# Kernel optimization log

Hardware: AMD Instinct MI355X
Metric: run time of the kernel (lower is better)

The kernel has to match this reference:

```python
import jax, jax.numpy as jnp
import numpy as np

N = 50000
NFEAT = 128
NHID = 64
EPS = 1e-5
NEG_SLOPE = 0.2


def gat_conv(x, src, dst, W, a_src, a_dst, b):
    # x: [N, in], W: [out, in], a_src/a_dst: [out], b: [out]
    h = x @ W.T                                   # [N, out]
    alpha_s = h @ a_src                           # [N]
    alpha_d = h @ a_dst                           # [N]
    e = jax.nn.leaky_relu(alpha_s[src] + alpha_d[dst], NEG_SLOPE)  # [E]
    # segment softmax over destination nodes
    m = jax.ops.segment_max(e, dst, num_segments=N)
    e = jnp.exp(e - m[dst])
    s = jax.ops.segment_sum(e, dst, num_segments=N)
    alpha = e / (s[dst] + 1e-16)
    out = jax.ops.segment_sum(alpha[:, None] * h[src], dst, num_segments=N)
    return out + b


def batch_norm(x, gamma, beta):
    mu = jnp.mean(x, axis=0)
    var = jnp.mean((x - mu) ** 2, axis=0)
    return gamma * (x - mu) * jax.lax.rsqrt(var + EPS) + beta


def setup_inputs() -> dict:
    key = jax.random.key(0)
    ks = jax.random.split(key, 24)
    E = 800000
    x = jax.random.normal(ks[0], (N, NFEAT), dtype=jnp.float32)
    edge_index = jax.random.randint(ks[1], (2, E), 0, N, dtype=jnp.int64)

    def lin(k, o, i):
        return jax.random.normal(k, (o, i), dtype=jnp.float32) / np.sqrt(i)

    def att(k, o):
        return jax.random.normal(k, (o,), dtype=jnp.float32) / np.sqrt(o)

    return dict(
        x=x, edge_index=edge_index,
        W1=lin(ks[2], NHID, NFEAT), a1s=att(ks[3], NHID), a1d=att(ks[4], NHID), b1=jnp.zeros((NHID,), jnp.float32),
        g1=jnp.ones((NHID,), jnp.float32), be1=jnp.zeros((NHID,), jnp.float32),
        W2=lin(ks[5], NHID, NHID), a2s=att(ks[6], NHID), a2d=att(ks[7], NHID), b2=jnp.zeros((NHID,), jnp.float32),
        g2=jnp.ones((NHID,), jnp.float32), be2=jnp.zeros((NHID,), jnp.float32),
        W3=lin(ks[8], NHID, NHID), a3s=att(ks[9], NHID), a3d=att(ks[10], NHID), b3=jnp.zeros((NHID,), jnp.float32),
        g3=jnp.ones((NHID,), jnp.float32), be3=jnp.zeros((NHID,), jnp.float32),
        W4=lin(ks[11], NFEAT, NHID), a4s=att(ks[12], NFEAT), a4d=att(ks[13], NFEAT), b4=jnp.zeros((NFEAT,), jnp.float32),
    )


def reference(x, edge_index, W1, a1s, a1d, b1, g1, be1, W2, a2s, a2d, b2, g2, be2,
              W3, a3s, a3d, b3, g3, be3, W4, a4s, a4d, b4):
    loops = jnp.arange(N, dtype=edge_index.dtype)
    src = jnp.concatenate([edge_index[0], loops])  # add self-loops (PyG default)
    dst = jnp.concatenate([edge_index[1], loops])
    # Encoder
    h = jax.nn.relu(gat_conv(x, src, dst, W1, a1s, a1d, b1))
    h = batch_norm(h, g1, be1)
    h = jax.nn.relu(gat_conv(h, src, dst, W2, a2s, a2d, b2))
    h = batch_norm(h, g2, be2)
    # Attribute decoder
    h = jax.nn.relu(gat_conv(h, src, dst, W3, a3s, a3d, b3))
    h = batch_norm(h, g3, be3)
    x_hat = jax.nn.relu(gat_conv(h, src, dst, W4, a4s, a4d, b4))
    diff = jnp.abs(x - x_hat)
    return diff, x_hat
```

## Files before the change

### kernel.cpp

```cpp
#include <hip/hip_runtime.h>
#include <math.h>

#define NND 50000
#define EPSB 1e-5f
#define SLOPE 0.2f
#define NB 256
#define SBLK 128
#define BRANGE 196

typedef float vfloat4 __attribute__((ext_vector_type(4)));

__device__ __forceinline__ float lrelu(float v) { return v > 0.f ? v : SLOPE * v; }

__device__ __forceinline__ ushort f2bf(float f) {
    unsigned u = __float_as_uint(f);
    unsigned r = (u + 0x7fffu + ((u >> 16) & 1u)) >> 16;
    return (ushort)r;
}

__device__ __forceinline__ void nt_store4(float4 v, float4* p) {
    vfloat4 t = {v.x, v.y, v.z, v.w};
    __builtin_nontemporal_store(t, (vfloat4*)p);
}

__device__ __forceinline__ void acc8(float* a, uint4 w, float e) {
    a[0] += e * __uint_as_float(w.x << 16);
    a[1] += e * __uint_as_float(w.x & 0xffff0000u);
    a[2] += e * __uint_as_float(w.y << 16);
    a[3] += e * __uint_as_float(w.y & 0xffff0000u);
    a[4] += e * __uint_as_float(w.z << 16);
    a[5] += e * __uint_as_float(w.z & 0xffff0000u);
    a[6] += e * __uint_as_float(w.w << 16);
    a[7] += e * __uint_as_float(w.w & 0xffff0000u);
}


__global__ __launch_bounds__(256) void countC_kernel(const int* __restrict__ ei, int E,
                                                     int* __restrict__ cnt, int* __restrict__ C) {
    __shared__ int lc[NB];
    const int tid = threadIdx.x;
    for (int i = tid; i < NB; i += 256) lc[i] = 0;
    __syncthreads();
    const int per = (E + SBLK - 1) / SBLK;
    const int beg = blockIdx.x * per;
    const int end = min(beg + per, E);
    for (int i = beg + tid; i < end; i += 256) {
        int d = __builtin_nontemporal_load(&ei[E + i]);
        atomicAdd(&cnt[d], 1);
        atomicAdd(&lc[d / BRANGE], 1);
    }
    __syncthreads();
    for (int i = tid; i < NB; i += 256) C[i * SBLK + blockIdx.x] = lc[i];
}

__global__ __launch_bounds__(1024) void scanC_kernel(int* __restrict__ C) {
    __shared__ int ps[1024];
    const int t = threadIdx.x;
    int v[NB * SBLK / 1024];
    int s = 0;
#pragma unroll
    for (int j = 0; j < NB * SBLK / 1024; j++) {
        v[j] = C[t * (NB * SBLK / 1024) + j];
        s += v[j];
    }
    ps[t] = s;
    __syncthreads();
    for (int off = 1; off < 1024; off <<= 1) {
        int x = (t >= off) ? ps[t - off] : 0;
        __syncthreads();
        ps[t] += x;
        __syncthreads();
    }
    int ex = ps[t] - s;
#pragma unroll
    for (int j = 0; j < NB * SBLK / 1024; j++) {
        int tmp = v[j];
        C[t * (NB * SBLK / 1024) + j] = ex;
        ex += tmp;
    }
}

__global__ __launch_bounds__(256) void scatter_pairs_kernel(const int* __restrict__ ei, int E,
                                                            const int* __restrict__ C,
                                                            unsigned long long* __restrict__ pairs) {
    __shared__ int woff[NB];
    const int tid = threadIdx.x;
    for (int i = tid; i < NB; i += 256) woff[i] = C[i * SBLK + blockIdx.x];
    __syncthreads();
    const int per = (E + SBLK - 1) / SBLK;
    const int beg = blockIdx.x * per;
    const int end = min(beg + per, E);
    for (int i = beg + tid; i < end; i += 256) {
        int s = __builtin_nontemporal_load(&ei[i]);
        int d = __builtin_nontemporal_load(&ei[E + i]);
        int p = atomicAdd(&woff[d / BRANGE], 1);
        pairs[p] = ((unsigned long long)(unsigned)d << 32) | (unsigned)s;
    }
}

__global__ void scan1_kernel(const int* __restrict__ in, int n, int* __restrict__ outex,
                             int* __restrict__ bsum) {
    __shared__ int tmp[256];
    int tid = threadIdx.x;
    int i = blockIdx.x * 256 + tid;
    int v = (i < n) ? in[i] + 1 : 0;
    tmp[tid] = v;
    __syncthreads();
    for (int off = 1; off < 256; off <<= 1) {
        int t = (tid >= off) ? tmp[tid - off] : 0;
        __syncthreads();
        tmp[tid] += t;
        __syncthreads();
    }
    if (i < n) outex[i] = tmp[tid] - v;
    if (tid == 255) bsum[blockIdx.x] = tmp[255];
}

__global__ void scan2_kernel(const int* __restrict__ in, int n, int* __restrict__ outex) {
    __shared__ int tmp[256];
    int tid = threadIdx.x;
    int v = (tid < n) ? in[tid] : 0;
    tmp[tid] = v;
    __syncthreads();
    for (int off = 1; off < 256; off <<= 1) {
        int t = (tid >= off) ? tmp[tid - off] : 0;
        __syncthreads();
        tmp[tid] += t;
        __syncthreads();
    }
    if (tid < n) outex[tid] = tmp[tid] - v;
}

__global__ void scan3_kernel(int* __restrict__ rp, const int* __restrict__ boff,
                             int* __restrict__ fill, int* __restrict__ srcs, int n, int etot) {
    int i = blockIdx.x * 256 + threadIdx.x;
    if (i < n) {
        int v = rp[i] + boff[blockIdx.x];
        rp[i] = v;
        srcs[v] = i;
        fill[i] = v + 1;
    }
    if (i == 0) rp[n] = etot;
}

__global__ __launch_bounds__(256) void bucket_csr_kernel(const unsigned long long* __restrict__ pairs,
                                                         int E, const int* __restrict__ C,
                                                         int* __restrict__ fill,
                                                         int* __restrict__ srcs) {
    const int b = blockIdx.x;
    const int beg = C[b * SBLK];
    const int end = (b == NB - 1) ? E : C[(b + 1) * SBLK];
    for (int i = beg + threadIdx.x; i < end; i += 256) {
        unsigned long long pr = __builtin_nontemporal_load(&pairs[i]);
        int d = (int)(pr >> 32);
        int s = (int)(pr & 0xffffffffu);
        int p = atomicAdd(&fill[d], 1);
        srcs[p] = s;
    }
}


template <int K, int FOUT>
__global__ __launch_bounds__(256) void gemm_kernel(
    const float* __restrict__ X, const float* __restrict__ W, ushort* __restrict__ H, int n,
    const float* __restrict__ bnsum, const float* __restrict__ bnsq, const float* __restrict__ g,
    const float* __restrict__ be, const float* __restrict__ asrc, const float* __restrict__ adst,
    float* __restrict__ as_o, float* __restrict__ ad_o) {
    constexpr int SW = FOUT + 4;
    constexpr int SX = 68;
    constexpr int NF = FOUT / 64;
    __shared__ float Wt[64 * SW];
    __shared__ float Xt[64 * SX];
    __shared__ float bnsc[K];
    __shared__ float bnsh[K];
    const int tid = threadIdx.x;
    const int nodeBase = blockIdx.x * 64;
    const int tx = tid & 15, ty = tid >> 4;
    const bool doBN = (bnsum != nullptr);

    if (doBN) {
        const float invn = 1.f / (float)NND;
        for (int f = tid; f < K; f += 256) {
            float mu = bnsum[f] * invn;
            float var = bnsq[f] * invn - mu * mu;
            float r = rsqrtf(var + EPSB);
            float sc = g[f] * r;
            bnsc[f] = sc;
            bnsh[f] = be[f] - mu * sc;
        }
    }
    __syncthreads();

    float acc[4][4 * NF];
#pragma unroll
    for (int i = 0; i < 4; i++)
#pragma unroll
        for (int j = 0; j < 4 * NF; j++) acc[i][j] = 0.f;

    for (int kc = 0; kc < K; kc += 64) {
        for (int idx = tid; idx < FOUT * 64; idx += 256) {
            int f = idx >> 6, kk = idx & 63;
            Wt[kk * SW + f] = W[f * K + kc + kk];
        }
        for (int idx = tid; idx < 64 * 16; idx += 256) {
            int r = idx >> 4, c4 = idx & 15;
            int node = nodeBase + r;
            float4 v = make_float4(0.f, 0.f, 0.f, 0.f);
            if (node < n) {
                v = ((const float4*)X)[node * (K / 4) + (kc >> 2) + c4];
                if (doBN) {
                    int f = kc + c4 * 4;
                    v.x = v.x * bnsc[f + 0] + bnsh[f + 0];
                    v.y = v.y * bnsc[f + 1] + bnsh[f + 1];
                    v.z = v.z * bnsc[f + 2] + bnsh[f + 2];
                    v.w = v.w * bnsc[f + 3] + bnsh[f + 3];
                }
            }
            Xt[(c4 * 4 + 0) * SX + r] = v.x;
            Xt[(c4 * 4 + 1) * SX + r] = v.y;
            Xt[(c4 * 4 + 2) * SX + r] = v.z;
            Xt[(c4 * 4 + 3) * SX + r] = v.w;
        }
        __syncthreads();
#pragma unroll 16
        for (int k = 0; k < 64; k++) {
            const float4 xv = *(const float4*)(Xt + k * SX + ty * 4);
            const float4 wv = *(const float4*)(Wt + k * SW + tx * 4);
            const float xa[4] = {xv.x, xv.y, xv.z, xv.w};
            float wa[4 * NF];
            wa[0] = wv.x; wa[1] = wv.y; wa[2] = wv.z; wa[3] = wv.w;
            if constexpr (NF == 2) {
                const float4 wv2 = *(const float4*)(Wt + k * SW + 64 + tx * 4);
                wa[4] = wv2.x; wa[5] = wv2.y; wa[6] = wv2.z; wa[7] = wv2.w;
            }
#pragma unroll
            for (int i = 0; i < 4; i++)
#pragma unroll
                for (int j = 0; j < 4 * NF; j++) acc[i][j] += xa[i] * wa[j];
        }
        __syncthreads();
    }
#pragma unroll
    for (int i = 0; i < 4; i++) {
        int node = nodeBase + ty * 4 + i;
        if (node < n) {
            ushort4 o;
            o.x = f2bf(acc[i][0]); o.y = f2bf(acc[i][1]);
            o.z = f2bf(acc[i][2]); o.w = f2bf(acc[i][3]);
            ((ushort4*)H)[node * (FOUT / 4) + tx] = o;
            if constexpr (NF == 2) {
                ushort4 o2;
                o2.x = f2bf(acc[i][4]); o2.y = f2bf(acc[i][5]);
                o2.z = f2bf(acc[i][6]); o2.w = f2bf(acc[i][7]);
                ((ushort4*)H)[node * (FOUT / 4) + 16 + tx] = o2;
            }
        }
    }
    if (as_o) {
        float asv[4 * NF], adv[4 * NF];
#pragma unroll
        for (int j = 0; j < 4; j++) {
            asv[j] = asrc[tx * 4 + j];
            adv[j] = adst[tx * 4 + j];
            if constexpr (NF == 2) {
                asv[4 + j] = asrc[64 + tx * 4 + j];
                adv[4 + j] = adst[64 + tx * 4 + j];
            }
        }
#pragma unroll
        for (int i = 0; i < 4; i++) {
            int node = nodeBase + ty * 4 + i;
            float ps = 0.f, pd = 0.f;
#pragma unroll
            for (int j = 0; j < 4 * NF; j++) {
                ps += acc[i][j] * asv[j];
                pd += acc[i][j] * adv[j];
            }
#pragma unroll
            for (int off = 1; off < 16; off <<= 1) {
                ps += __shfl_xor(ps, off, 64);
                pd += __shfl_xor(pd, off, 64);
            }
            if (tx == 0 && node < n) {
                as_o[node] = ps;
                ad_o[node] = pd;
            }
        }
    }
}


template <int F, bool FINAL>
__global__ __launch_bounds__(256) void edge_kernel(
    const int* __restrict__ rp, const int* __restrict__ srcs, const float* __restrict__ as_,
    const float* __restrict__ ad_, const ushort* __restrict__ h, const float* __restrict__ bias,
    float* __restrict__ y, float* __restrict__ bnsum, float* __restrict__ bnsq,
    const float* __restrict__ xin, float* __restrict__ odiff, float* __restrict__ oxhat) {
    constexpr int GS = F / 8;
    constexpr int GPW = 64 / GS;
    const int tid = threadIdx.x;
    const int lane = tid & 63;
    const int wslot = tid >> 6;
    const int sub = lane & (GS - 1);
    const int grp = (blockIdx.x * 4 + wslot) * GPW + lane / GS;
    const int ngrp = gridDim.x * 4 * GPW;
    const float4 bA = ((const float4*)bias)[sub * 2];
    const float4 bB = ((const float4*)bias)[sub * 2 + 1];
    float st[8], qt[8];
#pragma unroll
    for (int j = 0; j < 8; j++) st[j] = qt[j] = 0.f;

    for (int row = grp; row < NND; row += ngrp) {
        const int beg = rp[row], end = rp[row + 1];
        const float ad = ad_[row];
        float a[8];
#pragma unroll
        for (int j = 0; j < 8; j++) a[j] = 0.f;
        float sw = 0.f;
        int i = beg;
        for (; i + 4 <= end; i += 4) {
            int s0 = __builtin_nontemporal_load(&srcs[i]);
            int s1 = __builtin_nontemporal_load(&srcs[i + 1]);
            int s2 = __builtin_nontemporal_load(&srcs[i + 2]);
            int s3 = __builtin_nontemporal_load(&srcs[i + 3]);
            uint4 h0 = *(const uint4*)(h + (size_t)s0 * F + sub * 8);
            uint4 h1 = *(const uint4*)(h + (size_t)s1 * F + sub * 8);
            uint4 h2 = *(const uint4*)(h + (size_t)s2 * F + sub * 8);
            uint4 h3 = *(const uint4*)(h + (size_t)s3 * F + sub * 8);
            float e0 = __expf(fminf(lrelu(as_[s0] + ad), 80.f));
            float e1 = __expf(fminf(lrelu(as_[s1] + ad), 80.f));
            float e2 = __expf(fminf(lrelu(as_[s2] + ad), 80.f));
            float e3 = __expf(fminf(lrelu(as_[s3] + ad), 80.f));
            acc8(a, h0, e0);
            acc8(a, h1, e1);
            acc8(a, h2, e2);
            acc8(a, h3, e3);
            sw += (e0 + e1) + (e2 + e3);
        }
        for (; i < end; i++) {
            int s0 = __builtin_nontemporal_load(&srcs[i]);
            uint4 h0 = *(const uint4*)(h + (size_t)s0 * F + sub * 8);
            float e0 = __expf(fminf(lrelu(as_[s0] + ad), 80.f));
            acc8(a, h0, e0);
            sw += e0;
        }
        const float inv = 1.f / (sw + 1e-16f);
        float4 ya, yb;
        ya.x = fmaxf(a[0] * inv + bA.x, 0.f);
        ya.y = fmaxf(a[1] * inv + bA.y, 0.f);
        ya.z = fmaxf(a[2] * inv + bA.z, 0.f);
        ya.w = fmaxf(a[3] * inv + bA.w, 0.f);
        yb.x = fmaxf(a[4] * inv + bB.x, 0.f);
        yb.y = fmaxf(a[5] * inv + bB.y, 0.f);
        yb.z = fmaxf(a[6] * inv + bB.z, 0.f);
        yb.w = fmaxf(a[7] * inv + bB.w, 0.f);
        if constexpr (FINAL) {
            const float4* xr = (const float4*)(xin + (size_t)row * F);
            float4 xa = xr[sub * 2], xb = xr[sub * 2 + 1];
            float4* xo = (float4*)(oxhat + (size_t)row * F);
            nt_store4(ya, &xo[sub * 2]);
            nt_store4(yb, &xo[sub * 2 + 1]);
            float4 da, db;
            da.x = fabsf(xa.x - ya.x); da.y = fabsf(xa.y - ya.y);
            da.z = fabsf(xa.z - ya.z); da.w = fabsf(xa.w - ya.w);
            db.x = fabsf(xb.x - yb.x); db.y = fabsf(xb.y - yb.y);
            db.z = fabsf(xb.z - yb.z); db.w = fabsf(xb.w - yb.w);
            float4* dio = (float4*)(odiff + (size_t)row * F);
            nt_store4(da, &dio[sub * 2]);
            nt_store4(db, &dio[sub * 2 + 1]);
        } else {
            float4* yo = (float4*)(y + (size_t)row * F);
            nt_store4(ya, &yo[sub * 2]);
            nt_store4(yb, &yo[sub * 2 + 1]);
            st[0] += ya.x; qt[0] += ya.x * ya.x;
            st[1] += ya.y; qt[1] += ya.y * ya.y;
            st[2] += ya.z; qt[2] += ya.z * ya.z;
            st[3] += ya.w; qt[3] += ya.w * ya.w;
            st[4] += yb.x; qt[4] += yb.x * yb.x;
            st[5] += yb.y; qt[5] += yb.y * yb.y;
            st[6] += yb.z; qt[6] += yb.z * yb.z;
            st[7] += yb.w; qt[7] += yb.w * yb.w;
        }
    }
    if constexpr (!FINAL) {
        __shared__ float redS[256][8];
        __shared__ float redQ[256][8];
#pragma unroll
        for (int j = 0; j < 8; j++) {
            redS[tid][j] = st[j];
            redQ[tid][j] = qt[j];
        }
        __syncthreads();
        if (tid < F) {
            int sb = tid >> 3, j = tid & 7;
            float ts = 0.f, tq = 0.f;
            for (int k = 0; k < 256 / GS; k++) {
                int t2 = k * GS + sb;
                ts += redS[t2][j];
                tq += redQ[t2][j];
            }
            atomicAdd(&bnsum[tid], ts);
            atomicAdd(&bnsq[tid], tq);
        }
    }
}


extern "C" void kernel_launch(void* const* d_in, const int* in_sizes, int n_in, void* d_out,
                              int out_size, void* d_ws, size_t ws_size, hipStream_t stream) {
    const float* x = (const float*)d_in[0];
    const int* ei = (const int*)d_in[1];
    const int E = in_sizes[1] / 2;
    const float* W1 = (const float*)d_in[2];
    const float* a1s = (const float*)d_in[3];
    const float* a1d = (const float*)d_in[4];
    const float* b1 = (const float*)d_in[5];
    const float* g1 = (const float*)d_in[6];
    const float* be1 = (const float*)d_in[7];
    const float* W2 = (const float*)d_in[8];
    const float* a2s = (const float*)d_in[9];
    const float* a2d = (const float*)d_in[10];
    const float* b2 = (const float*)d_in[11];
    const float* g2 = (const float*)d_in[12];
    const float* be2 = (const float*)d_in[13];
    const float* W3 = (const float*)d_in[14];
    const float* a3s = (const float*)d_in[15];
    const float* a3d = (const float*)d_in[16];
    const float* b3 = (const float*)d_in[17];
    const float* g3 = (const float*)d_in[18];
    const float* be3 = (const float*)d_in[19];
    const float* W4 = (const float*)d_in[20];
    const float* a4s = (const float*)d_in[21];
    const float* a4d = (const float*)d_in[22];
    const float* b4 = (const float*)d_in[23];

    const int Etot = E + NND;

    char* w = (char*)d_ws;
    auto alloc = [&](size_t bytes) {
        void* p = (void*)w;
        w += (bytes + 255) & ~(size_t)255;
        return p;
    };
    int* cnt = (int*)alloc((size_t)NND * 4);
    float* stats = (float*)alloc(384 * 4);
    int* rp = (int*)alloc((size_t)(NND + 1) * 4);
    int* fill = (int*)alloc((size_t)NND * 4);
    int* bsum = (int*)alloc(256 * 4);
    int* bsum2 = (int*)alloc(256 * 4);
    int* C = (int*)alloc((size_t)NB * SBLK * 4);
    unsigned long long* pairs = (unsigned long long*)alloc((size_t)E * 8);
    int* srcs = (int*)alloc((size_t)Etot * 4);
    ushort* bufH = (ushort*)alloc((size_t)NND * 128 * 2);
    float* bufY = (float*)alloc((size_t)NND * 64 * 4);
    float* asb = (float*)alloc((size_t)NND * 4);
    float* adb = (float*)alloc((size_t)NND * 4);

    const int nblk = (NND + 255) / 256;
    const int ggrid = (NND + 63) / 64;
    const int xgrid = 2048;

    hipError_t _e = hipMemsetAsync(cnt, 0, (((size_t)NND * 4 + 255) & ~(size_t)255) + 384 * 4, stream);
    (void)_e;

    countC_kernel<<<SBLK, 256, 0, stream>>>(ei, E, cnt, C);
    scan1_kernel<<<nblk, 256, 0, stream>>>(cnt, NND, rp, bsum);
    scan2_kernel<<<1, 256, 0, stream>>>(bsum, nblk, bsum2);
    scan3_kernel<<<nblk, 256, 0, stream>>>(rp, bsum2, fill, srcs, NND, Etot);
    scanC_kernel<<<1, 1024, 0, stream>>>(C);
    scatter_pairs_kernel<<<SBLK, 256, 0, stream>>>(ei, E, C, pairs);
    bucket_csr_kernel<<<NB, 256, 0, stream>>>(pairs, E, C, fill, srcs);

    gemm_kernel<128, 64><<<ggrid, 256, 0, stream>>>(x, W1, bufH, NND, nullptr, nullptr, nullptr,
                                                    nullptr, a1s, a1d, asb, adb);
    edge_kernel<64, false><<<xgrid, 256, 0, stream>>>(rp, srcs, asb, adb, bufH, b1, bufY,
                                                      stats + 0, stats + 64, nullptr, nullptr,
                                                      nullptr);
    gemm_kernel<64, 64><<<ggrid, 256, 0, stream>>>(bufY, W2, bufH, NND, stats + 0, stats + 64,
                                                   g1, be1, a2s, a2d, asb, adb);
    edge_kernel<64, false><<<xgrid, 256, 0, stream>>>(rp, srcs, asb, adb, bufH, b2, bufY,
                                                      stats + 128, stats + 192, nullptr, nullptr,
                                                      nullptr);
    gemm_kernel<64, 64><<<ggrid, 256, 0, stream>>>(bufY, W3, bufH, NND, stats + 128, stats + 192,
                                                   g2, be2, a3s, a3d, asb, adb);
    edge_kernel<64, false><<<xgrid, 256, 0, stream>>>(rp, srcs, asb, adb, bufH, b3, bufY,
                                                      stats + 256, stats + 320, nullptr, nullptr,
                                                      nullptr);
    float* odiff = (float*)d_out;
    float* oxhat = (float*)d_out + (size_t)NND * 128;
    gemm_kernel<64, 128><<<ggrid, 256, 0, stream>>>(bufY, W4, bufH, NND, stats + 256, stats + 320,
                                                    g3, be3, a4s, a4d, asb, adb);
    edge_kernel<128, true><<<xgrid, 256, 0, stream>>>(rp, srcs, asb, adb, bufH, b4, nullptr,
                                                      nullptr, nullptr, x, odiff, oxhat);
}
```

Baseline: 547.6 us.

## Drop nontemporal hints, replace memset with zero kernel, halve edge grid

Non-temporal loads of the CSR source indices and non-temporal stores of activations and outputs become ordinary cached accesses. The hipMemsetAsync is replaced by a small custom kernel that zeroes the counts and BN stats, and the edge kernel grid drops from 2048 to 1024 blocks. Bounds clamps are added to the scatter write positions as a safety guard. The changes trade streaming cache hints for normal caching, cut launch and API overhead, and reduce per-block reduction overhead, at the cost of less latency hiding in the edge kernel.

Measured after the change: 454.0 us. -17.1%, faster.

```diff
diff --git a/kernel.cpp b/kernel.cpp
--- a/kernel.cpp
+++ b/kernel.cpp
@@ -8,19 +8,12 @@
 #define SBLK 128
 #define BRANGE 196
 
-typedef float vfloat4 __attribute__((ext_vector_type(4)));
-
 __device__ __forceinline__ float lrelu(float v) { return v > 0.f ? v : SLOPE * v; }
 
 __device__ __forceinline__ ushort f2bf(float f) {
     unsigned u = __float_as_uint(f);
     unsigned r = (u + 0x7fffu + ((u >> 16) & 1u)) >> 16;
     return (ushort)r;
-}
-
-__device__ __forceinline__ void nt_store4(float4 v, float4* p) {
-    vfloat4 t = {v.x, v.y, v.z, v.w};
-    __builtin_nontemporal_store(t, (vfloat4*)p);
 }
 
 __device__ __forceinline__ void acc8(float* a, uint4 w, float e) {
@@ -34,6 +27,12 @@
     a[7] += e * __uint_as_float(w.w & 0xffff0000u);
 }
 
+__global__ void zero_kernel(int* __restrict__ cnt, float* __restrict__ stats) {
+    int i = blockIdx.x * 256 + threadIdx.x;
+    if (i < NND) cnt[i] = 0;
+    if (i < 384) stats[i] = 0.f;
+}
+
 
 __global__ __launch_bounds__(256) void countC_kernel(const int* __restrict__ ei, int E,
                                                      int* __restrict__ cnt, int* __restrict__ C) {
@@ -94,6 +93,7 @@
         int s = __builtin_nontemporal_load(&ei[i]);
         int d = __builtin_nontemporal_load(&ei[E + i]);
         int p = atomicAdd(&woff[d / BRANGE], 1);
+        p = min(p, E - 1);
         pairs[p] = ((unsigned long long)(unsigned)d << 32) | (unsigned)s;
     }
 }
@@ -144,7 +144,7 @@
 }
 
 __global__ __launch_bounds__(256) void bucket_csr_kernel(const unsigned long long* __restrict__ pairs,
-                                                         int E, const int* __restrict__ C,
+                                                         int E, int etot, const int* __restrict__ C,
                                                          int* __restrict__ fill,
                                                          int* __restrict__ srcs) {
     const int b = blockIdx.x;
@@ -155,6 +155,7 @@
         int d = (int)(pr >> 32);
         int s = (int)(pr & 0xffffffffu);
         int p = atomicAdd(&fill[d], 1);
+        p = min(p, etot - 1);
         srcs[p] = s;
     }
 }
@@ -319,10 +320,7 @@
         float sw = 0.f;
         int i = beg;
         for (; i + 4 <= end; i += 4) {
-            int s0 = __builtin_nontemporal_load(&srcs[i]);
-            int s1 = __builtin_nontemporal_load(&srcs[i + 1]);
-            int s2 = __builtin_nontemporal_load(&srcs[i + 2]);
-            int s3 = __builtin_nontemporal_load(&srcs[i + 3]);
+            int s0 = srcs[i], s1 = srcs[i + 1], s2 = srcs[i + 2], s3 = srcs[i + 3];
             uint4 h0 = *(const uint4*)(h + (size_t)s0 * F + sub * 8);
             uint4 h1 = *(const uint4*)(h + (size_t)s1 * F + sub * 8);
             uint4 h2 = *(const uint4*)(h + (size_t)s2 * F + sub * 8);
@@ -338,7 +336,7 @@
             sw += (e0 + e1) + (e2 + e3);
         }
         for (; i < end; i++) {
-            int s0 = __builtin_nontemporal_load(&srcs[i]);
+            int s0 = srcs[i];
             uint4 h0 = *(const uint4*)(h + (size_t)s0 * F + sub * 8);
             float e0 = __expf(fminf(lrelu(as_[s0] + ad), 80.f));
             acc8(a, h0, e0);
@@ -358,20 +356,20 @@
             const float4* xr = (const float4*)(xin + (size_t)row * F);
             float4 xa = xr[sub * 2], xb = xr[sub * 2 + 1];
             float4* xo = (float4*)(oxhat + (size_t)row * F);
-            nt_store4(ya, &xo[sub * 2]);
-            nt_store4(yb, &xo[sub * 2 + 1]);
+            xo[sub * 2] = ya;
+            xo[sub * 2 + 1] = yb;
             float4 da, db;
             da.x = fabsf(xa.x - ya.x); da.y = fabsf(xa.y - ya.y);
             da.z = fabsf(xa.z - ya.z); da.w = fabsf(xa.w - ya.w);
             db.x = fabsf(xb.x - yb.x); db.y = fabsf(xb.y - yb.y);
             db.z = fabsf(xb.z - yb.z); db.w = fabsf(xb.w - yb.w);
             float4* dio = (float4*)(odiff + (size_t)row * F);
-            nt_store4(da, &dio[sub * 2]);
-            nt_store4(db, &dio[sub * 2 + 1]);
+            dio[sub * 2] = da;
+            dio[sub * 2 + 1] = db;
         } else {
             float4* yo = (float4*)(y + (size_t)row * F);
-            nt_store4(ya, &yo[sub * 2]);
-            nt_store4(yb, &yo[sub * 2 + 1]);
+            yo[sub * 2] = ya;
+            yo[sub * 2 + 1] = yb;
             st[0] += ya.x; qt[0] += ya.x * ya.x;
             st[1] += ya.y; qt[1] += ya.y * ya.y;
             st[2] += ya.z; qt[2] += ya.z * ya.z;
@@ -458,18 +456,16 @@
 
     const int nblk = (NND + 255) / 256;
     const int ggrid = (NND + 63) / 64;
-    const int xgrid = 2048;
-
-    hipError_t _e = hipMemsetAsync(cnt, 0, (((size_t)NND * 4 + 255) & ~(size_t)255) + 384 * 4, stream);
-    (void)_e;
-
+    const int xgrid = 1024;
+
+    zero_kernel<<<nblk, 256, 0, stream>>>(cnt, stats);
     countC_kernel<<<SBLK, 256, 0, stream>>>(ei, E, cnt, C);
     scan1_kernel<<<nblk, 256, 0, stream>>>(cnt, NND, rp, bsum);
     scan2_kernel<<<1, 256, 0, stream>>>(bsum, nblk, bsum2);
     scan3_kernel<<<nblk, 256, 0, stream>>>(rp, bsum2, fill, srcs, NND, Etot);
     scanC_kernel<<<1, 1024, 0, stream>>>(C);
     scatter_pairs_kernel<<<SBLK, 256, 0, stream>>>(ei, E, C, pairs);
-    bucket_csr_kernel<<<NB, 256, 0, stream>>>(pairs, E, C, fill, srcs);
+    bucket_csr_kernel<<<NB, 256, 0, stream>>>(pairs, E, Etot, C, fill, srcs);
 
     gemm_kernel<128, 64><<<ggrid, 256, 0, stream>>>(x, W1, bufH, NND, nullptr, nullptr, nullptr,
                                                     nullptr, a1s, a1d, asb, adb);
```
